# Kernel tuning notes

Measured on AMD Instinct MI355X. Metric: run time of the kernel, lower is better.

The kernel has to match this reference:

```python
import jax, jax.numpy as jnp
import numpy as np

L, B, T, F, C, H, DFF = 2, 4, 2048, 1024, 200, 8, 128


def setup_inputs() -> dict:
    key = jax.random.key(0)
    ks = jax.random.split(key, 12)
    s = 0.02
    return {
        "x": jax.random.normal(ks[0], (B, T, F), jnp.float32),
        "prototypes": jax.random.normal(ks[1], (C, 1, F), jnp.float32),
        # conv_query / conv_key (1x1 convs == linear), per RAB layer
        "wq": jax.random.normal(ks[2], (L, F, F), jnp.float32) * s,
        "bq": jnp.zeros((L, F), jnp.float32),
        "wk": jax.random.normal(ks[3], (L, F, F), jnp.float32) * s,
        "bk": jnp.zeros((L, F), jnp.float32),
        # nn.MultiheadAttention packed in-proj and out-proj
        "in_w": jax.random.normal(ks[4], (L, 3 * F, F), jnp.float32) * s,
        "in_b": jnp.zeros((L, 3 * F), jnp.float32),
        "out_w": jax.random.normal(ks[5], (L, F, F), jnp.float32) * s,
        "out_b": jnp.zeros((L, F), jnp.float32),
        # FFN
        "l1_w": jax.random.normal(ks[6], (L, DFF, F), jnp.float32) * s,
        "l1_b": jnp.zeros((L, DFF), jnp.float32),
        "l2_w": jax.random.normal(ks[7], (L, F, DFF), jnp.float32) * s,
        "l2_b": jnp.zeros((L, F), jnp.float32),
        # LayerNorms
        "ln1_g": jnp.ones((L, F), jnp.float32),
        "ln1_b": jnp.zeros((L, F), jnp.float32),
        "ln2_g": jnp.ones((L, F), jnp.float32),
        "ln2_b": jnp.zeros((L, F), jnp.float32),
        # feature_embedding: Conv1d(F, F, k=3, pad=1) + ReLU
        "emb_w": jax.random.normal(ks[8], (F, F, 3), jnp.float32) * s,
        "emb_b": jnp.zeros((F,), jnp.float32),
    }


def _ln(x, g, b, eps=1e-5):
    mu = jnp.mean(x, axis=-1, keepdims=True)
    var = jnp.mean((x - mu) ** 2, axis=-1, keepdims=True)
    return (x - mu) * jax.lax.rsqrt(var + eps) * g + b


def _mha(q, k, v, w, b, ow, ob):
    # q,k,v: (B,S,F). Packed in-proj like nn.MultiheadAttention (eval: no dropout).
    f = q.shape[-1]
    dh = f // H
    Q = q @ w[:f].T + b[:f]
    K = k @ w[f:2 * f].T + b[f:2 * f]
    V = v @ w[2 * f:].T + b[2 * f:]
    sp = lambda t: t.reshape(t.shape[0], t.shape[1], H, dh)
    scale = np.float32(1.0 / np.sqrt(dh))
    att = jnp.einsum('bqhd,bkhd->bhqk', sp(Q), sp(K)) * scale
    att = jax.nn.softmax(att, axis=-1)
    o = jnp.einsum('bhqk,bkhd->bqhd', att, sp(V)).reshape(q.shape)
    return o @ ow.T + ob


def reference(x, prototypes, wq, bq, wk, bk, in_w, in_b, out_w, out_b,
              l1_w, l1_b, l2_w, l2_b, ln1_g, ln1_b, ln2_g, ln2_b, emb_w, emb_b):
    Bn, Tn, Fn = x.shape
    # torch: prototypes.view(1, F, -1)  (a reshape, NOT a transpose)
    proto = jnp.broadcast_to(prototypes.reshape(1, Fn, -1), (Bn, Fn, prototypes.shape[0]))
    # concat along time: (B,F,S) with S = T + C, then work in (B,S,F)
    src = jnp.swapaxes(jnp.concatenate([jnp.swapaxes(x, 1, 2), proto], axis=2), 1, 2)
    for l in range(L):
        q = src @ wq[l].T + bq[l]          # conv1x1 == pointwise linear
        k = src @ wk[l].T + bk[l]
        a = _mha(q, k, src, in_w[l], in_b[l], out_w[l], out_b[l])
        src = _ln(src + a, ln1_g[l], ln1_b[l])
        ff = jax.nn.relu(src @ l1_w[l].T + l1_b[l]) @ l2_w[l].T + l2_b[l]
        src = _ln(src + ff, ln2_g[l], ln2_b[l])
    feat = jnp.swapaxes(src[:, :Tn], 1, 2)  # (B,F,T): drop prototype tokens
    y = jax.lax.conv_general_dilated(feat, emb_w, (1,), ((1, 1),),
                                     dimension_numbers=('NCH', 'OIH', 'NCH'))
    return jax.nn.relu(y + emb_b[None, :, None])
```

## Files before the change

### kernel.cpp

```cpp
#include <hip/hip_runtime.h>
#include <hip/hip_bf16.h>


constexpr int BN = 4, TN = 2048, FD = 1024, CP = 200, SN = TN + CP;
constexpr int HN = 8, DH = 128, DF = 128, MR = BN * SN;
constexpr int SF = 3 * FD;
constexpr int NT = (SN + 63) / 64;
constexpr float C2 = 0.12751744f;

typedef __attribute__((ext_vector_type(8))) short short8;
typedef __attribute__((ext_vector_type(4))) float f32x4;

__device__ __forceinline__ ushort f2b(float f) {
  union { float f; uint u; } v{f};
  return (ushort)((v.u + 0x7fffu + ((v.u >> 16) & 1u)) >> 16);
}
__device__ __forceinline__ float b2f(ushort u) {
  union { uint u; float f; } v{(uint)u << 16};
  return v.f;
}
__device__ __forceinline__ uint cvt_pk_bf16(float a, float b) {
  uint r;
  asm("v_cvt_pk_bf16_f32 %0, %1, %2" : "=v"(r) : "v"(a), "v"(b));
  return r;
}
__device__ __forceinline__ float exp2_fast(float x) {
  float r;
  asm("v_exp_f32 %0, %1" : "=v"(r) : "v"(x));
  return r;
}
__device__ __forceinline__ void gld16(const void* g, void* l) {
  __builtin_amdgcn_global_load_lds(
      (const __attribute__((address_space(1))) void*)g,
      (__attribute__((address_space(3))) void*)l, 16, 0, 0);
}

__global__ __launch_bounds__(256) void k_build(const float* __restrict__ x,
                                               const float* __restrict__ proto,
                                               ushort* __restrict__ srcb) {
  const int row = blockIdx.x;
  const int b = row / SN, s = row % SN;
  const int f = threadIdx.x * 4;
  const size_t o = (size_t)row * FD + f;
  float4 v;
  if (s < TN) {
    v = *(const float4*)(x + ((size_t)b * TN + s) * FD + f);
  } else {
    const int c = s - TN;
    v.x = proto[(size_t)(f + 0) * CP + c];
    v.y = proto[(size_t)(f + 1) * CP + c];
    v.z = proto[(size_t)(f + 2) * CP + c];
    v.w = proto[(size_t)(f + 3) * CP + c];
  }
  ushort4 u{f2b(v.x), f2b(v.y), f2b(v.z), f2b(v.w)};
  *(ushort4*)(srcb + o) = u;
}

__global__ __launch_bounds__(256) void k_cvt(const float* __restrict__ in,
                                             ushort* __restrict__ out, int n) {
  const int n4 = n >> 2;
  for (int i = blockIdx.x * 256 + threadIdx.x; i < n4; i += gridDim.x * 256) {
    const float4 v = *(const float4*)(in + (size_t)i * 4);
    ushort4 u{f2b(v.x), f2b(v.y), f2b(v.z), f2b(v.w)};
    *(ushort4*)(out + (size_t)i * 4) = u;
  }
}

__global__ __launch_bounds__(256) void k_cvt_inw(const float* __restrict__ in,
                                                 ushort* __restrict__ wInQK,
                                                 ushort* __restrict__ wQKV) {
  constexpr size_t FF = (size_t)FD * FD;
  const int n4 = (int)(6 * FF / 4);
  for (int i = blockIdx.x * 256 + threadIdx.x; i < n4; i += gridDim.x * 256) {
    const size_t idx = (size_t)i * 4;
    const float4 v = *(const float4*)(in + idx);
    ushort4 u{f2b(v.x), f2b(v.y), f2b(v.z), f2b(v.w)};
    const int l = (int)(idx / (3 * FF));
    const size_t r = idx % (3 * FF);
    ushort* dst = (r >= 2 * FF) ? (wQKV + l * 3 * FF + r)
                                : (wInQK + l * 2 * FF + r);
    *(ushort4*)dst = u;
  }
}

__global__ __launch_bounds__(256) void k_cvtT(const float* __restrict__ wq,
                                              const float* __restrict__ wk,
                                              ushort* __restrict__ wT) {
  const int z = blockIdx.z;
  const int qk = z >> 1, l = z & 1;
  const float* W = (qk ? wk : wq) + (size_t)l * FD * FD;
  ushort* WT = wT + (size_t)z * FD * FD;
  __shared__ float t[32][33];
  const int tx = threadIdx.x & 31, ty = threadIdx.x >> 5;
  const int x0 = blockIdx.x * 32, y0 = blockIdx.y * 32;
#pragma unroll
  for (int dy = 0; dy < 4; ++dy)
    t[ty + dy * 8][tx] = W[(size_t)(y0 + ty + dy * 8) * FD + x0 + tx];
  __syncthreads();
#pragma unroll
  for (int dy = 0; dy < 4; ++dy)
    WT[(size_t)(x0 + ty + dy * 8) * FD + y0 + tx] = f2b(t[tx][ty + dy * 8]);
}

__global__ __launch_bounds__(256) void k_vT(const ushort* __restrict__ V,
                                            ushort* __restrict__ Vt) {
  __shared__ ushort t[32][34];
  const int tx = threadIdx.x & 31, ty = threadIdx.x >> 5;
  const int s0 = blockIdx.x * 32, d0 = blockIdx.y * 32, bh = blockIdx.z;
  const int b = bh >> 3, h = bh & 7;
#pragma unroll
  for (int dy = 0; dy < 4; ++dy) {
    const int s = min(s0 + ty + dy * 8, SN - 1);
    t[ty + dy * 8][tx] = V[((size_t)b * SN + s) * SF + h * DH + d0 + tx];
  }
  __syncthreads();
#pragma unroll
  for (int dy = 0; dy < 4; ++dy) {
    const int s = s0 + tx;
    if (s < SN)
      Vt[((size_t)bh * DH + d0 + ty + dy * 8) * SN + s] = t[tx][ty + dy * 8];
  }
}

__global__ __launch_bounds__(256) void k_convw(const float* __restrict__ W,
                                               ushort* __restrict__ out) {
  const int n = FD * FD * 3;
  for (int idx = blockIdx.x * 256 + threadIdx.x; idx < n;
       idx += gridDim.x * 256) {
    const int o = idx / (FD * 3);
    const int rem = idx % (FD * 3);
    const int tau = rem >> 10, i = rem & 1023;
    out[idx] = f2b(W[(size_t)o * (FD * 3) + i * 3 + tau]);
  }
}

__global__ __launch_bounds__(256) void k_pad(const ushort* __restrict__ sb,
                                             ushort* __restrict__ pad) {
  const int r = blockIdx.x, b = blockIdx.y;
  const int f = threadIdx.x * 4;
  ushort4 v{0, 0, 0, 0};
  if (r >= 1 && r <= TN)
    v = *(const ushort4*)(sb + ((size_t)b * SN + (r - 1)) * FD + f);
  *(ushort4*)(pad + ((size_t)b * (TN + 2) + r) * FD + f) = v;
}

__global__ __launch_bounds__(256) void k_beff(const float* __restrict__ in_w,
                                              const float* __restrict__ bq,
                                              const float* __restrict__ bk,
                                              const float* __restrict__ in_b,
                                              float* __restrict__ out) {
  const int n = blockIdx.x, l = blockIdx.y, qk = blockIdx.z;
  const int tid = threadIdx.x;
  if (qk == 2) {
    if (tid == 0)
      out[l * 3 * FD + 2 * FD + n] = in_b[l * 3 * FD + 2 * FD + n];
    return;
  }
  const float* Win = in_w + (size_t)(l * 3 + qk) * FD * FD;
  const float* bv = (qk ? bk : bq) + (size_t)l * FD;
  float s = 0.f;
  for (int j = tid; j < FD; j += 256) s += Win[(size_t)n * FD + j] * bv[j];
  __shared__ float red[4];
#pragma unroll
  for (int o = 32; o; o >>= 1) s += __shfl_xor(s, o);
  if ((tid & 63) == 0) red[tid >> 6] = s;
  __syncthreads();
  if (tid == 0)
    out[l * 3 * FD + qk * FD + n] =
        red[0] + red[1] + red[2] + red[3] + in_b[l * 3 * FD + qk * FD + n];
}

template <bool RELU, bool BF16OUT, bool PREP4 = false>
__global__ __launch_bounds__(256) void k_mm(const ushort* __restrict__ A,
                                            const ushort* __restrict__ W,
                                            const float* __restrict__ bias,
                                            void* __restrict__ Cv,
                                            int M, int N, int K) {
  constexpr size_t FF = (size_t)FD * FD;
  if (PREP4) {
    const int z = blockIdx.z;
    A += (size_t)z * FF;
    W += (size_t)(((z & 1) * 2) + (z >> 1)) * FF;
    Cv = (void*)((ushort*)Cv + (size_t)((z >> 1) * 3 + (z & 1)) * FF);
  }
  __shared__ __align__(16) ushort As[128 * 32];
  __shared__ __align__(16) ushort Ws[128 * 32];
  const int tid = threadIdx.x;
  const int lane = tid & 63, wv = tid >> 6;
  const int l15 = lane & 15, g = lane >> 4;
  const int wr = wv >> 1, wc = wv & 1;
  int bx = blockIdx.x, by = blockIdx.y;
  const int nwg = gridDim.x * gridDim.y;
  if ((nwg & 7) == 0) {
    int bid = by * gridDim.x + bx;
    bid = (bid & 7) * (nwg >> 3) + (bid >> 3);
    bx = bid % gridDim.x;
    by = bid / gridDim.x;
  }
  const int m0 = by * 128, n0 = bx * 128;
  f32x4 acc[4][4];
#pragma unroll
  for (int i = 0; i < 4; ++i)
#pragma unroll
    for (int j = 0; j < 4; ++j) acc[i][j] = (f32x4){0.f, 0.f, 0.f, 0.f};

  for (int k0 = 0; k0 < K; k0 += 32) {
#pragma unroll
    for (int j = 0; j < 2; ++j) {
      const int u = j * 256 + wv * 64 + lane;
      const int r = u >> 2, c = (u & 3) * 8;
      const int gm = min(m0 + r, M - 1);
      gld16(A + (size_t)gm * K + k0 + c, As + (size_t)u * 8);
    }
#pragma unroll
    for (int j = 0; j < 2; ++j) {
      const int u = j * 256 + wv * 64 + lane;
      const int r = u >> 2, c = (u & 3) * 8;
      gld16(W + (size_t)(n0 + r) * K + k0 + c, Ws + (size_t)u * 8);
    }
    __syncthreads();
    short8 af[4], bfr[4];
#pragma unroll
    for (int i = 0; i < 4; ++i)
      af[i] = *(const short8*)(As + (wr * 64 + i * 16 + l15) * 32 + g * 8);
#pragma unroll
    for (int j = 0; j < 4; ++j)
      bfr[j] = *(const short8*)(Ws + (wc * 64 + j * 16 + l15) * 32 + g * 8);
    __builtin_amdgcn_s_setprio(1);
#pragma unroll
    for (int i = 0; i < 4; ++i)
#pragma unroll
      for (int j = 0; j < 4; ++j)
        acc[i][j] = __builtin_amdgcn_mfma_f32_16x16x32_bf16(af[i], bfr[j],
                                                            acc[i][j], 0, 0, 0);
    __builtin_amdgcn_s_setprio(0);
    __syncthreads();
  }
#pragma unroll
  for (int i = 0; i < 4; ++i) {
#pragma unroll
    for (int r = 0; r < 4; ++r) {
      const int row = m0 + wr * 64 + i * 16 + g * 4 + r;
      if (row >= M) continue;
#pragma unroll
      for (int j = 0; j < 4; ++j) {
        const int col = n0 + wc * 64 + j * 16 + l15;
        float v = acc[i][j][r];
        if (bias) v += bias[col];
        if (RELU) v = fmaxf(v, 0.f);
        if (BF16OUT)
          ((ushort*)Cv)[(size_t)row * N + col] = f2b(v);
        else
          ((float*)Cv)[(size_t)row * N + col] = v;
      }
    }
  }
}

template <bool CONV, bool BF16OUT>
__global__ __launch_bounds__(512, 1) void k_mmB(const ushort* __restrict__ A,
                                                const ushort* __restrict__ W,
                                                const float* __restrict__ bias,
                                                void* __restrict__ Cv,
                                                int M, int N, int K) {
  __shared__ __align__(16) ushort As[2][128 * 64];
  __shared__ __align__(16) ushort Bs[2][256 * 64];
  const int tid = threadIdx.x;
  const int lane = tid & 63, wv = tid >> 6;
  const int l15 = lane & 15, g = lane >> 4;
  const int wr = wv >> 2, wc = wv & 3;
  int bx = blockIdx.x, by = blockIdx.y;
  const int nwg = gridDim.x * gridDim.y;
  if ((nwg & 7) == 0) {
    int bid = by * gridDim.x + bx;
    bid = (bid & 7) * (nwg >> 3) + (bid >> 3);
    bx = bid % gridDim.x;
    by = bid / gridDim.x;
  }
  const int m0 = by * 128, n0 = bx * 256;
  const int NKt = K >> 6;

  f32x4 acc[4][4];
#pragma unroll
  for (int i = 0; i < 4; ++i)
#pragma unroll
    for (int j = 0; j < 4; ++j) acc[i][j] = (f32x4){0.f, 0.f, 0.f, 0.f};

  auto stage = [&](int kt, int d) {
    const int kb = kt * 64;
#pragma unroll
    for (int j = 0; j < 2; ++j) {
      const int u = j * 512 + tid;
      const int row = u >> 3, s = u & 7;
      const int c = s ^ (row & 7);
      const ushort* ga;
      if (CONV) {
        const int rm = m0 + row;
        const int bb = rm >> 11, tt = rm & 2047;
        ga = A + (size_t)(bb * (TN + 2) + tt + (kb >> 10)) * FD + (kb & 1023) +
             c * 8;
      } else {
        ga = A + (size_t)min(m0 + row, M - 1) * K + kb + c * 8;
      }
      gld16(ga, As[d] + row * 64 + s * 8);
    }
#pragma unroll
    for (int j = 0; j < 4; ++j) {
      const int u = j * 512 + tid;
      const int row = u >> 3, s = u & 7;
      const int c = s ^ (row & 7);
      gld16(W + (size_t)(n0 + row) * K + kb + c * 8, Bs[d] + row * 64 + s * 8);
    }
  };

  stage(0, 0);
  for (int kt = 0; kt < NKt; ++kt) {
    const int cur = kt & 1;
    if (kt + 1 < NKt) {
      stage(kt + 1, cur ^ 1);
      asm volatile("s_waitcnt vmcnt(6)" ::: "memory");
    } else {
      asm volatile("s_waitcnt vmcnt(0)" ::: "memory");
    }
    __builtin_amdgcn_s_barrier();
    __builtin_amdgcn_sched_barrier(0);
#pragma unroll
    for (int ks = 0; ks < 2; ++ks) {
      short8 aq[4], bq[4];
#pragma unroll
      for (int mf = 0; mf < 4; ++mf) {
        const int row = wr * 64 + mf * 16 + l15;
        aq[mf] = *(const short8*)(As[cur] + row * 64 +
                                  (((ks * 4 + g) ^ (row & 7)) << 3));
      }
#pragma unroll
      for (int nf = 0; nf < 4; ++nf) {
        const int row = wc * 64 + nf * 16 + l15;
        bq[nf] = *(const short8*)(Bs[cur] + row * 64 +
                                  (((ks * 4 + g) ^ (row & 7)) << 3));
      }
      __builtin_amdgcn_s_setprio(1);
#pragma unroll
      for (int mf = 0; mf < 4; ++mf)
#pragma unroll
        for (int nf = 0; nf < 4; ++nf)
          acc[mf][nf] = __builtin_amdgcn_mfma_f32_16x16x32_bf16(
              aq[mf], bq[nf], acc[mf][nf], 0, 0, 0);
      __builtin_amdgcn_s_setprio(0);
    }
    asm volatile("s_waitcnt lgkmcnt(0)" ::: "memory");
    __builtin_amdgcn_s_barrier();
  }

#pragma unroll
  for (int mf = 0; mf < 4; ++mf) {
#pragma unroll
    for (int r = 0; r < 4; ++r) {
      const int row = m0 + wr * 64 + mf * 16 + g * 4 + r;
      if (!CONV && row >= M) continue;
#pragma unroll
      for (int nf = 0; nf < 4; ++nf) {
        const int col = n0 + wc * 64 + nf * 16 + l15;
        float v = acc[mf][nf][r];
        if (bias) v += bias[col];
        if (CONV) {
          v = fmaxf(v, 0.f);
          const int bb = row >> 11, tt = row & 2047;
          ((float*)Cv)[((size_t)(bb * FD + col)) * TN + tt] = v;
        } else if (BF16OUT) {
          ((ushort*)Cv)[(size_t)row * N + col] = f2b(v);
        } else {
          ((float*)Cv)[(size_t)row * N + col] = v;
        }
      }
    }
  }
}

__global__ __launch_bounds__(512) void k_fattn(const ushort* __restrict__ Qg,
                                               const ushort* __restrict__ Kg,
                                               const ushort* __restrict__ Vt,
                                               ushort* __restrict__ Og) {
  __shared__ __align__(16) ushort Ks[2][64 * 128];
  __shared__ __align__(16) ushort Vs[2][128 * 64];
  __shared__ __align__(16) ushort Ps[8][16 * 64];
  const int tid = threadIdx.x, lane = tid & 63, wv = tid >> 6;
  const int l15 = lane & 15, g = lane >> 4;
  const int b = blockIdx.z, h = blockIdx.y, q0 = blockIdx.x * 128;
  const size_t rowBase = (size_t)b * SN;
  const int hoff = h * DH;
  const size_t vbase = (size_t)(b * HN + h) * DH * SN;

  short8 qf[4];
  const int qrow = min(q0 + wv * 16 + l15, SN - 1);
#pragma unroll
  for (int c = 0; c < 4; ++c)
    qf[c] = *(const short8*)(Qg + (rowBase + qrow) * SF + hoff + c * 32 + g * 8);
  asm volatile("s_waitcnt vmcnt(0)" ::: "memory");

  short8 onesf;
#pragma unroll
  for (int i = 0; i < 8; ++i) onesf[i] = (short)0x3F80;

  f32x4 o[8];
#pragma unroll
  for (int dt = 0; dt < 8; ++dt) o[dt] = (f32x4){0.f, 0.f, 0.f, 0.f};
  f32x4 lacc = (f32x4){0.f, 0.f, 0.f, 0.f};
  char* PsB = (char*)&Ps[wv][0];

  auto stageK = [&](int kv0, ushort* dst, bool tail) {
#pragma unroll
    for (int j = 0; j < 2; ++j) {
      const int su = j * 512 + tid;
      const int row = su >> 4, s = su & 15;
      const int c16 = s ^ (row & 7);
      const int krow = tail ? min(kv0 + row, SN - 1) : kv0 + row;
      gld16(Kg + (rowBase + krow) * SF + hoff + c16 * 8, dst + (size_t)su * 8);
    }
  };
  auto stageV = [&](int kv0, ushort* dst, bool tail) {
#pragma unroll
    for (int j = 0; j < 2; ++j) {
      const int su = j * 512 + tid;
      const int row = su >> 3, s = su & 7;
      const int cc = s ^ (row & 7);
      const int kvc = tail ? min(kv0 + cc * 8, SN - 8) : kv0 + cc * 8;
      gld16(Vt + vbase + (size_t)row * SN + kvc, dst + (size_t)su * 8);
    }
  };

  stageK(0, Ks[0], false);
  stageV(0, Vs[0], false);

  for (int t = 0; t < NT; ++t) {
    const int kv0 = t * 64;
    const int cur = t & 1;
    if (t + 1 < NT) {
      const bool tl2 = (t + 1 == NT - 1);
      stageK(kv0 + 64, Ks[cur ^ 1], tl2);
      stageV(kv0 + 64, Vs[cur ^ 1], tl2);
      asm volatile("s_waitcnt vmcnt(4)" ::: "memory");
    } else {
      asm volatile("s_waitcnt vmcnt(0)" ::: "memory");
    }
    __builtin_amdgcn_s_barrier();
    __builtin_amdgcn_sched_barrier(0);
    const char* KsB = (const char*)Ks[cur];
    const char* VsB = (const char*)Vs[cur];

    f32x4 st[4];
    __builtin_amdgcn_s_setprio(1);
#pragma unroll
    for (int kt = 0; kt < 4; ++kt) {
      f32x4 s4 = (f32x4){0.f, 0.f, 0.f, 0.f};
      const int row = kt * 16 + l15;
#pragma unroll
      for (int c = 0; c < 4; ++c) {
        const short8 kf = *(const short8*)(
            KsB + row * 256 + (((c * 4 + g) ^ (row & 7)) << 4));
        s4 = __builtin_amdgcn_mfma_f32_16x16x32_bf16(kf, qf[c], s4, 0, 0, 0);
      }
      st[kt] = s4;
    }
    __builtin_amdgcn_s_setprio(0);

    float pfl[16];
    if (t == NT - 1) {
#pragma unroll
      for (int kt = 0; kt < 4; ++kt)
#pragma unroll
        for (int r = 0; r < 4; ++r) {
          const int kvg = kv0 + kt * 16 + g * 4 + r;
          pfl[kt * 4 + r] = (kvg < SN) ? exp2_fast(C2 * st[kt][r]) : 0.f;
        }
    } else {
#pragma unroll
      for (int i = 0; i < 16; ++i)
        pfl[i] = exp2_fast(C2 * st[i >> 2][i & 3]);
    }

#pragma unroll
    for (int kt = 0; kt < 4; ++kt) {
      const uint lo = cvt_pk_bf16(pfl[kt * 4 + 0], pfl[kt * 4 + 1]);
      const uint hi = cvt_pk_bf16(pfl[kt * 4 + 2], pfl[kt * 4 + 3]);
      const int slot = (kt * 2 + (g >> 1)) ^ (l15 & 7);
      *(uint2*)(PsB + l15 * 128 + slot * 16 + (g & 1) * 8) = make_uint2(lo, hi);
    }

    __builtin_amdgcn_s_setprio(1);
#pragma unroll
    for (int c2 = 0; c2 < 2; ++c2) {
      const int pslot = (c2 * 4 + g) ^ (l15 & 7);
      const short8 pf = *(const short8*)(PsB + l15 * 128 + pslot * 16);
      lacc = __builtin_amdgcn_mfma_f32_16x16x32_bf16(pf, onesf, lacc, 0, 0, 0);
#pragma unroll
      for (int dt = 0; dt < 8; ++dt) {
        const int row = dt * 16 + l15;
        const short8 vf = *(const short8*)(
            VsB + row * 128 + (((c2 * 4 + g) ^ (row & 7)) << 4));
        o[dt] = __builtin_amdgcn_mfma_f32_16x16x32_bf16(pf, vf, o[dt], 0, 0, 0);
      }
    }
    __builtin_amdgcn_s_setprio(0);
    asm volatile("s_waitcnt lgkmcnt(0)" ::: "memory");
    __builtin_amdgcn_s_barrier();
  }

  float ir[4];
#pragma unroll
  for (int r = 0; r < 4; ++r) ir[r] = 1.f / lacc[r];
#pragma unroll
  for (int r = 0; r < 4; ++r) {
    const int orow = q0 + wv * 16 + g * 4 + r;
    if (orow >= SN) continue;
#pragma unroll
    for (int dt = 0; dt < 8; ++dt)
      Og[(rowBase + orow) * FD + hoff + dt * 16 + l15] = f2b(o[dt][r] * ir[r]);
  }
}

__global__ __launch_bounds__(256) void k_add_ln(ushort* __restrict__ sb,
                                                const ushort* __restrict__ d,
                                                const float* __restrict__ g,
                                                const float* __restrict__ be) {
  __shared__ float red[4];
  const int row = blockIdx.x;
  const int tid = threadIdx.x;
  const int c = tid * 4;
  const size_t off = (size_t)row * FD + c;
  const ushort4 sv = *(const ushort4*)(sb + off);
  const ushort4 dv = *(const ushort4*)(d + off);
  float v[4] = {b2f(sv.x) + b2f(dv.x), b2f(sv.y) + b2f(dv.y),
                b2f(sv.z) + b2f(dv.z), b2f(sv.w) + b2f(dv.w)};
  float sum = v[0] + v[1] + v[2] + v[3];
#pragma unroll
  for (int o = 32; o; o >>= 1) sum += __shfl_xor(sum, o);
  if ((tid & 63) == 0) red[tid >> 6] = sum;
  __syncthreads();
  sum = red[0] + red[1] + red[2] + red[3];
  const float mu = sum * (1.f / FD);
  float vs = 0.f;
#pragma unroll
  for (int i = 0; i < 4; ++i) {
    const float t = v[i] - mu;
    vs += t * t;
  }
  __syncthreads();
#pragma unroll
  for (int o = 32; o; o >>= 1) vs += __shfl_xor(vs, o);
  if ((tid & 63) == 0) red[tid >> 6] = vs;
  __syncthreads();
  vs = red[0] + red[1] + red[2] + red[3];
  const float rstd = rsqrtf(vs * (1.f / FD) + 1e-5f);
  const float4 gv = *(const float4*)(g + c);
  const float4 bv = *(const float4*)(be + c);
  ushort4 u{f2b((v[0] - mu) * rstd * gv.x + bv.x),
            f2b((v[1] - mu) * rstd * gv.y + bv.y),
            f2b((v[2] - mu) * rstd * gv.z + bv.z),
            f2b((v[3] - mu) * rstd * gv.w + bv.w)};
  *(ushort4*)(sb + off) = u;
}

extern "C" void kernel_launch(void* const* d_in, const int* in_sizes, int n_in,
                              void* d_out, int out_size, void* d_ws,
                              size_t ws_size, hipStream_t stream) {
  const float* x      = (const float*)d_in[0];
  const float* proto  = (const float*)d_in[1];
  const float* wq     = (const float*)d_in[2];
  const float* bq     = (const float*)d_in[3];
  const float* wk     = (const float*)d_in[4];
  const float* bk     = (const float*)d_in[5];
  const float* in_w   = (const float*)d_in[6];
  const float* in_b   = (const float*)d_in[7];
  const float* out_w  = (const float*)d_in[8];
  const float* out_b  = (const float*)d_in[9];
  const float* l1_w   = (const float*)d_in[10];
  const float* l1_b   = (const float*)d_in[11];
  const float* l2_w   = (const float*)d_in[12];
  const float* l2_b   = (const float*)d_in[13];
  const float* ln1_g  = (const float*)d_in[14];
  const float* ln1_b  = (const float*)d_in[15];
  const float* ln2_g  = (const float*)d_in[16];
  const float* ln2_b  = (const float*)d_in[17];
  const float* emb_w  = (const float*)d_in[18];
  const float* emb_b  = (const float*)d_in[19];

  char* p = (char*)d_ws;
  auto take = [&](size_t bytes) {
    char* r = p;
    p += (bytes + 255) & ~(size_t)255;
    return r;
  };
  const size_t MF = (size_t)MR * FD;
  const size_t FF = (size_t)FD * FD;
  ushort* srcb  = (ushort*)take(MF * 2);
  ushort* bQKV  = (ushort*)take((size_t)MR * SF * 2);
  ushort* bVt   = (ushort*)take((size_t)BN * HN * DH * SN * 2);
  ushort* bO    = (ushort*)take(MF * 2);
  ushort* bFF   = (ushort*)take((size_t)MR * DF * 2);
  ushort* wQKV  = (ushort*)take((size_t)2 * 3 * FF * 2);
  ushort* wOut  = (ushort*)take((size_t)2 * FF * 2);
  ushort* wL1   = (ushort*)take((size_t)2 * DF * FD * 2);
  ushort* wL2   = (ushort*)take((size_t)2 * FD * DF * 2);
  float*  bqkv  = (float*)take((size_t)2 * SF * 4);
  ushort* wT     = bQKV;
  ushort* wInQK  = bQKV + 4 * FF;
  ushort* bOut   = bQKV;
  ushort* srcPad = bQKV;
  ushort* convW  = bQKV + (size_t)10 * 1024 * 1024;

  k_build<<<MR, 256, 0, stream>>>(x, proto, srcb);
  k_cvt_inw<<<2048, 256, 0, stream>>>(in_w, wInQK, wQKV);
  k_cvt<<<1024, 256, 0, stream>>>(out_w, wOut, 2 * FF);
  k_cvt<<<256, 256, 0, stream>>>(l1_w, wL1, 2 * DF * FD);
  k_cvt<<<256, 256, 0, stream>>>(l2_w, wL2, 2 * FD * DF);
  k_cvtT<<<dim3(32, 32, 4), 256, 0, stream>>>(wq, wk, wT);
  k_mm<false, true, true><<<dim3(8, 8, 4), 256, 0, stream>>>(
      wInQK, wT, nullptr, wQKV, FD, FD, FD);
  k_beff<<<dim3(FD, 2, 3), 256, 0, stream>>>(in_w, bq, bk, in_b, bqkv);

  const int MB = (MR + 127) / 128;

  for (int l = 0; l < 2; ++l) {
    k_mmB<false, true><<<dim3(SF / 256, MB), 512, 0, stream>>>(
        srcb, wQKV + (size_t)l * 3 * FF, bqkv + (size_t)l * SF, bQKV, MR, SF,
        FD);
    k_vT<<<dim3((SN + 31) / 32, DH / 32, BN * HN), 256, 0, stream>>>(
        bQKV + 2 * FD, bVt);
    k_fattn<<<dim3((SN + 127) / 128, HN, BN), 512, 0, stream>>>(
        bQKV, bQKV + FD, bVt, bO);
    k_mmB<false, true><<<dim3(FD / 256, MB), 512, 0, stream>>>(
        bO, wOut + (size_t)l * FF, out_b + (size_t)l * FD, bOut, MR, FD, FD);
    k_add_ln<<<MR, 256, 0, stream>>>(srcb, bOut, ln1_g + (size_t)l * FD,
                                     ln1_b + (size_t)l * FD);
    k_mm<true, true><<<dim3(DF / 128, MB), 256, 0, stream>>>(
        srcb, wL1 + (size_t)l * DF * FD, l1_b + (size_t)l * DF, bFF, MR, DF,
        FD);
    k_mm<false, true><<<dim3(FD / 128, MB), 256, 0, stream>>>(
        bFF, wL2 + (size_t)l * FD * DF, l2_b + (size_t)l * FD, bOut, MR, FD,
        DF);
    k_add_ln<<<MR, 256, 0, stream>>>(srcb, bOut, ln2_g + (size_t)l * FD,
                                     ln2_b + (size_t)l * FD);
  }

  k_convw<<<1024, 256, 0, stream>>>(emb_w, convW);
  k_pad<<<dim3(TN + 2, BN), 256, 0, stream>>>(srcb, srcPad);
  k_mmB<true, false><<<dim3(FD / 256, (BN * TN) / 128), 512, 0, stream>>>(
      srcPad, convW, emb_b, (float*)d_out, BN * TN, FD, 3 * FD);
}
```

Baseline: 971.3 us.

## Rewrite flash attention with 32x32 MFMA tiles and four-wave blocks

Result: no change. 987.5 us (+1.7%).

```diff
diff --git a/kernel.cpp b/kernel.cpp
--- a/kernel.cpp
+++ b/kernel.cpp
@@ -10,6 +10,7 @@
 
 typedef __attribute__((ext_vector_type(8))) short short8;
 typedef __attribute__((ext_vector_type(4))) float f32x4;
+typedef __attribute__((ext_vector_type(16))) float f32x16;
 
 __device__ __forceinline__ ushort f2b(float f) {
   union { float f; uint u; } v{f};
@@ -377,145 +378,127 @@
   }
 }
 
-__global__ __launch_bounds__(512) void k_fattn(const ushort* __restrict__ Qg,
+__global__ __launch_bounds__(256) void k_fattn(const ushort* __restrict__ Qg,
                                                const ushort* __restrict__ Kg,
                                                const ushort* __restrict__ Vt,
                                                ushort* __restrict__ Og) {
-  __shared__ __align__(16) ushort Ks[2][64 * 128];
-  __shared__ __align__(16) ushort Vs[2][128 * 64];
-  __shared__ __align__(16) ushort Ps[8][16 * 64];
+  __shared__ __align__(16) ushort Ks[64 * 128];
+  __shared__ __align__(16) ushort Vs[128 * 64];
+  __shared__ __align__(16) ushort Ps[4][32 * 64];
   const int tid = threadIdx.x, lane = tid & 63, wv = tid >> 6;
-  const int l15 = lane & 15, g = lane >> 4;
+  const int l31 = lane & 31, hh = lane >> 5;
   const int b = blockIdx.z, h = blockIdx.y, q0 = blockIdx.x * 128;
   const size_t rowBase = (size_t)b * SN;
   const int hoff = h * DH;
   const size_t vbase = (size_t)(b * HN + h) * DH * SN;
 
-  short8 qf[4];
-  const int qrow = min(q0 + wv * 16 + l15, SN - 1);
-#pragma unroll
-  for (int c = 0; c < 4; ++c)
-    qf[c] = *(const short8*)(Qg + (rowBase + qrow) * SF + hoff + c * 32 + g * 8);
-  asm volatile("s_waitcnt vmcnt(0)" ::: "memory");
-
-  short8 onesf;
-#pragma unroll
-  for (int i = 0; i < 8; ++i) onesf[i] = (short)0x3F80;
-
-  f32x4 o[8];
-#pragma unroll
-  for (int dt = 0; dt < 8; ++dt) o[dt] = (f32x4){0.f, 0.f, 0.f, 0.f};
-  f32x4 lacc = (f32x4){0.f, 0.f, 0.f, 0.f};
+  short8 qf[8];
+  const int qrow = min(q0 + wv * 32 + l31, SN - 1);
+#pragma unroll
+  for (int ks = 0; ks < 8; ++ks)
+    qf[ks] = *(const short8*)(Qg + (rowBase + qrow) * SF + hoff + ks * 16 +
+                              hh * 8);
+
+  f32x16 o[4];
+#pragma unroll
+  for (int dn = 0; dn < 4; ++dn)
+#pragma unroll
+    for (int r = 0; r < 16; ++r) o[dn][r] = 0.f;
+  float lacc = 0.f;
+  const char* KsB = (const char*)Ks;
+  const char* VsB = (const char*)Vs;
   char* PsB = (char*)&Ps[wv][0];
 
-  auto stageK = [&](int kv0, ushort* dst, bool tail) {
-#pragma unroll
-    for (int j = 0; j < 2; ++j) {
-      const int su = j * 512 + tid;
+  for (int t = 0; t < NT; ++t) {
+    const int kv0 = t * 64;
+    const bool tl = (t == NT - 1);
+#pragma unroll
+    for (int j = 0; j < 4; ++j) {
+      const int su = j * 256 + tid;
       const int row = su >> 4, s = su & 15;
-      const int c16 = s ^ (row & 7);
-      const int krow = tail ? min(kv0 + row, SN - 1) : kv0 + row;
-      gld16(Kg + (rowBase + krow) * SF + hoff + c16 * 8, dst + (size_t)su * 8);
-    }
-  };
-  auto stageV = [&](int kv0, ushort* dst, bool tail) {
-#pragma unroll
-    for (int j = 0; j < 2; ++j) {
-      const int su = j * 512 + tid;
+      const int c16 = s ^ (row & 15);
+      const int krow = tl ? min(kv0 + row, SN - 1) : kv0 + row;
+      gld16(Kg + (rowBase + krow) * SF + hoff + c16 * 8, Ks + (size_t)su * 8);
+    }
+#pragma unroll
+    for (int j = 0; j < 4; ++j) {
+      const int su = j * 256 + tid;
       const int row = su >> 3, s = su & 7;
       const int cc = s ^ (row & 7);
-      const int kvc = tail ? min(kv0 + cc * 8, SN - 8) : kv0 + cc * 8;
-      gld16(Vt + vbase + (size_t)row * SN + kvc, dst + (size_t)su * 8);
-    }
-  };
-
-  stageK(0, Ks[0], false);
-  stageV(0, Vs[0], false);
-
-  for (int t = 0; t < NT; ++t) {
-    const int kv0 = t * 64;
-    const int cur = t & 1;
-    if (t + 1 < NT) {
-      const bool tl2 = (t + 1 == NT - 1);
-      stageK(kv0 + 64, Ks[cur ^ 1], tl2);
-      stageV(kv0 + 64, Vs[cur ^ 1], tl2);
-      asm volatile("s_waitcnt vmcnt(4)" ::: "memory");
-    } else {
-      asm volatile("s_waitcnt vmcnt(0)" ::: "memory");
-    }
-    __builtin_amdgcn_s_barrier();
-    __builtin_amdgcn_sched_barrier(0);
-    const char* KsB = (const char*)Ks[cur];
-    const char* VsB = (const char*)Vs[cur];
-
-    f32x4 st[4];
+      const int kvc = tl ? min(kv0 + cc * 8, SN - 8) : kv0 + cc * 8;
+      gld16(Vt + vbase + (size_t)row * SN + kvc, Vs + (size_t)su * 8);
+    }
+    __syncthreads();
+
+    f32x16 st0, st1;
+#pragma unroll
+    for (int r = 0; r < 16; ++r) { st0[r] = 0.f; st1[r] = 0.f; }
     __builtin_amdgcn_s_setprio(1);
 #pragma unroll
-    for (int kt = 0; kt < 4; ++kt) {
-      f32x4 s4 = (f32x4){0.f, 0.f, 0.f, 0.f};
-      const int row = kt * 16 + l15;
-#pragma unroll
-      for (int c = 0; c < 4; ++c) {
-        const short8 kf = *(const short8*)(
-            KsB + row * 256 + (((c * 4 + g) ^ (row & 7)) << 4));
-        s4 = __builtin_amdgcn_mfma_f32_16x16x32_bf16(kf, qf[c], s4, 0, 0, 0);
-      }
-      st[kt] = s4;
+    for (int ks = 0; ks < 8; ++ks) {
+      const int slot = (ks * 2 + hh) ^ (l31 & 15);
+      const short8 kf0 = *(const short8*)(KsB + l31 * 256 + slot * 16);
+      const short8 kf1 = *(const short8*)(KsB + (32 + l31) * 256 + slot * 16);
+      st0 = __builtin_amdgcn_mfma_f32_32x32x16_bf16(kf0, qf[ks], st0, 0, 0, 0);
+      st1 = __builtin_amdgcn_mfma_f32_32x32x16_bf16(kf1, qf[ks], st1, 0, 0, 0);
     }
     __builtin_amdgcn_s_setprio(0);
 
-    float pfl[16];
-    if (t == NT - 1) {
-#pragma unroll
-      for (int kt = 0; kt < 4; ++kt)
-#pragma unroll
-        for (int r = 0; r < 4; ++r) {
-          const int kvg = kv0 + kt * 16 + g * 4 + r;
-          pfl[kt * 4 + r] = (kvg < SN) ? exp2_fast(C2 * st[kt][r]) : 0.f;
+    auto smax = [&](const f32x16& stv, int mt) {
+      float pfl[16];
+      if (tl) {
+#pragma unroll
+        for (int r = 0; r < 16; ++r) {
+          const int kvg = kv0 + mt * 32 + (r & 3) + 8 * (r >> 2) + 4 * hh;
+          pfl[r] = (kvg < SN) ? exp2_fast(C2 * stv[r]) : 0.f;
         }
-    } else {
-#pragma unroll
-      for (int i = 0; i < 16; ++i)
-        pfl[i] = exp2_fast(C2 * st[i >> 2][i & 3]);
-    }
-
-#pragma unroll
-    for (int kt = 0; kt < 4; ++kt) {
-      const uint lo = cvt_pk_bf16(pfl[kt * 4 + 0], pfl[kt * 4 + 1]);
-      const uint hi = cvt_pk_bf16(pfl[kt * 4 + 2], pfl[kt * 4 + 3]);
-      const int slot = (kt * 2 + (g >> 1)) ^ (l15 & 7);
-      *(uint2*)(PsB + l15 * 128 + slot * 16 + (g & 1) * 8) = make_uint2(lo, hi);
-    }
+      } else {
+#pragma unroll
+        for (int r = 0; r < 16; ++r) pfl[r] = exp2_fast(C2 * stv[r]);
+      }
+      float ls = 0.f;
+#pragma unroll
+      for (int r = 0; r < 16; ++r) ls += pfl[r];
+      lacc += ls;
+#pragma unroll
+      for (int gg = 0; gg < 4; ++gg) {
+        const uint lo = cvt_pk_bf16(pfl[4 * gg + 0], pfl[4 * gg + 1]);
+        const uint hi = cvt_pk_bf16(pfl[4 * gg + 2], pfl[4 * gg + 3]);
+        const int slot = (mt * 4 + gg) ^ (l31 & 7);
+        *(uint2*)(PsB + l31 * 128 + slot * 16 + hh * 8) = make_uint2(lo, hi);
+      }
+    };
+    smax(st0, 0);
+    smax(st1, 1);
 
     __builtin_amdgcn_s_setprio(1);
 #pragma unroll
-    for (int c2 = 0; c2 < 2; ++c2) {
-      const int pslot = (c2 * 4 + g) ^ (l15 & 7);
-      const short8 pf = *(const short8*)(PsB + l15 * 128 + pslot * 16);
-      lacc = __builtin_amdgcn_mfma_f32_16x16x32_bf16(pf, onesf, lacc, 0, 0, 0);
-#pragma unroll
-      for (int dt = 0; dt < 8; ++dt) {
-        const int row = dt * 16 + l15;
-        const short8 vf = *(const short8*)(
-            VsB + row * 128 + (((c2 * 4 + g) ^ (row & 7)) << 4));
-        o[dt] = __builtin_amdgcn_mfma_f32_16x16x32_bf16(pf, vf, o[dt], 0, 0, 0);
+    for (int ks = 0; ks < 4; ++ks) {
+      const int pslot = ((ks << 1) | hh) ^ (l31 & 7);
+      const short8 pf = *(const short8*)(PsB + l31 * 128 + pslot * 16);
+#pragma unroll
+      for (int dn = 0; dn < 4; ++dn) {
+        const int vrow = dn * 32 + l31;
+        const int vslot = ((ks << 1) | hh) ^ (vrow & 7);
+        const short8 vf = *(const short8*)(VsB + vrow * 128 + vslot * 16);
+        o[dn] = __builtin_amdgcn_mfma_f32_32x32x16_bf16(pf, vf, o[dn], 0, 0, 0);
       }
     }
     __builtin_amdgcn_s_setprio(0);
-    asm volatile("s_waitcnt lgkmcnt(0)" ::: "memory");
-    __builtin_amdgcn_s_barrier();
-  }
-
-  float ir[4];
-#pragma unroll
-  for (int r = 0; r < 4; ++r) ir[r] = 1.f / lacc[r];
-#pragma unroll
-  for (int r = 0; r < 4; ++r) {
-    const int orow = q0 + wv * 16 + g * 4 + r;
+    __syncthreads();
+  }
+
+  lacc += __shfl_xor(lacc, 32);
+  const float ir_self = 1.f / lacc;
+#pragma unroll
+  for (int r = 0; r < 16; ++r) {
+    const int ql = (r & 3) + 8 * (r >> 2) + 4 * hh;
+    const float ir = __shfl(ir_self, ql);
+    const int orow = q0 + wv * 32 + ql;
     if (orow >= SN) continue;
 #pragma unroll
-    for (int dt = 0; dt < 8; ++dt)
-      Og[(rowBase + orow) * FD + hoff + dt * 16 + l15] = f2b(o[dt][r] * ir[r]);
+    for (int dn = 0; dn < 4; ++dn)
+      Og[(rowBase + orow) * FD + hoff + dn * 32 + l31] = f2b(o[dn][r] * ir);
   }
 }
 
@@ -627,7 +610,7 @@
         FD);
     k_vT<<<dim3((SN + 31) / 32, DH / 32, BN * HN), 256, 0, stream>>>(
         bQKV + 2 * FD, bVt);
-    k_fattn<<<dim3((SN + 127) / 128, HN, BN), 512, 0, stream>>>(
+    k_fattn<<<dim3((SN + 127) / 128, HN, BN), 256, 0, stream>>>(
         bQKV, bQKV + FD, bVt, bO);
     k_mmB<false, true><<<dim3(FD / 256, MB), 512, 0, stream>>>(
         bO, wOut + (size_t)l * FF, out_b + (size_t)l * FD, bOut, MR, FD, FD);
```
